# Kernel optimization log

Measured on AMD Instinct MI355X. Metric: run time of the kernel, lower is better.

## Reference

```python
import jax, jax.numpy as jnp
import numpy as np

N = 50000
E = 600000
H = 128
LN_EPS = 1e-5


def _layer_norm(h, g, b):
    mu = jnp.mean(h, axis=-1, keepdims=True)
    var = jnp.var(h, axis=-1, keepdims=True)
    return (h - mu) * jax.lax.rsqrt(var + LN_EPS) * g + b


def _mlp(h, params):
    # params = (w0, b0, w1, b1, w2, b2, ln_g, ln_b); mlp_layers=2 pattern:
    # Linear->ReLU->Linear->ReLU->Linear->LayerNorm
    w0, b0, w1, b1, w2, b2, g, be = params
    h = jax.nn.relu(h @ w0 + b0)
    h = jax.nn.relu(h @ w1 + b1)
    h = h @ w2 + b2
    return _layer_norm(h, g, be)


def setup_inputs() -> dict:
    key = jax.random.key(0)
    ks = jax.random.split(key, 16)
    def lin(k, fan_in, fan_out):
        lim = 1.0 / np.sqrt(fan_in)
        kw, kb = jax.random.split(k)
        w = jax.random.uniform(kw, (fan_in, fan_out), jnp.float32, -lim, lim)
        b = jax.random.uniform(kb, (fan_out,), jnp.float32, -lim, lim)
        return w, b
    x = jax.random.normal(ks[0], (N, H), jnp.float32)
    e = jax.random.normal(ks[1], (E, H), jnp.float32)
    edge_index = jax.random.randint(ks[2], (2, E), 0, N, jnp.int64)
    we0, be0 = lin(ks[3], 3 * H, H)
    we1, be1 = lin(ks[4], H, H)
    we2, be2 = lin(ks[5], H, H)
    wn0, bn0 = lin(ks[6], 2 * H, H)
    wn1, bn1 = lin(ks[7], H, H)
    wn2, bn2 = lin(ks[8], H, H)
    return {
        "x": x, "e": e, "edge_index": edge_index,
        "we0": we0, "be0": be0, "we1": we1, "be1": be1, "we2": we2, "be2": be2,
        "ge": jnp.ones((H,), jnp.float32), "bge": jnp.zeros((H,), jnp.float32),
        "wn0": wn0, "bn0": bn0, "wn1": wn1, "bn1": bn1, "wn2": wn2, "bn2": bn2,
        "gn": jnp.ones((H,), jnp.float32), "bgn": jnp.zeros((H,), jnp.float32),
    }


def reference(x, e, edge_index,
              we0, be0, we1, be1, we2, be2, ge, bge,
              wn0, bn0, wn1, bn1, wn2, bn2, gn, bgn):
    src = edge_index[0]
    dst = edge_index[1]
    # gather node feats per edge -> [E, 3H] -> edge MLP -> [E, H]
    edge_in = jnp.concatenate([x[dst], x[src], e], axis=-1)
    e_new = _mlp(edge_in, (we0, be0, we1, be1, we2, be2, ge, bge))
    # scatter-add edge messages into destination nodes -> [N, H]
    agg = jax.ops.segment_sum(e_new, dst, num_segments=x.shape[0])
    node_in = jnp.concatenate([x, agg], axis=-1)
    x_new = x + _mlp(node_in, (wn0, bn0, wn1, bn1, wn2, bn2, gn, bgn))
    return (x_new, e_new)
```

## Files before the change

kernel.cpp:

```cpp
#include <hip/hip_runtime.h>

#define NN 50000
#define NE 600000
#define HD 128

typedef __attribute__((ext_vector_type(8))) short short8;
typedef __attribute__((ext_vector_type(4))) float floatx4;

__device__ __forceinline__ unsigned short f2bf(float f) {
  unsigned int u = __builtin_bit_cast(unsigned int, f);
  u += 0x7FFFu + ((u >> 16) & 1u);
  return (unsigned short)(u >> 16);
}

__device__ __forceinline__ short8 cvt8(const float* __restrict__ p) {
  floatx4 v0 = *(const floatx4*)p;
  floatx4 v1 = *(const floatx4*)(p + 4);
  short8 r;
  r[0] = (short)f2bf(v0[0]); r[1] = (short)f2bf(v0[1]);
  r[2] = (short)f2bf(v0[2]); r[3] = (short)f2bf(v0[3]);
  r[4] = (short)f2bf(v1[0]); r[5] = (short)f2bf(v1[1]);
  r[6] = (short)f2bf(v1[2]); r[7] = (short)f2bf(v1[3]);
  return r;
}

__global__ void pack_w(const float* __restrict__ w, unsigned short* __restrict__ wp,
                       int total) {
  int p = blockIdx.x * blockDim.x + threadIdx.x;
  if (p >= total) return;
  int j = p & 7, lane = (p >> 3) & 63, t = p >> 9;
  int n0 = t & 7, k0 = t >> 3;
  int k = k0 * 32 + (lane >> 4) * 8 + j;
  int n = n0 * 16 + (lane & 15);
  wp[p] = f2bf(w[k * HD + n]);
}

__global__ void cvt_bf16(const float* __restrict__ in,
                         unsigned short* __restrict__ out, int total8) {
  int p = blockIdx.x * blockDim.x + threadIdx.x;
  if (p >= total8) return;
  short8 r = cvt8(in + (size_t)p * 8);
  *(short8*)(out + (size_t)p * 8) = r;
}

template <int KSTEPS>
__device__ __forceinline__ void gemm_tile(const unsigned short* a_base, int a_stride,
                                          const unsigned short* __restrict__ wp,
                                          int lane, floatx4* acc) {
  int quad = lane >> 4, l16 = lane & 15;
  for (int k0 = 0; k0 < KSTEPS; ++k0) {
    short8 a = *(const short8*)(a_base + l16 * a_stride + k0 * 32 + quad * 8);
    const unsigned short* w = wp + k0 * 4096 + lane * 8;
#pragma unroll
    for (int n0 = 0; n0 < 8; ++n0) {
      short8 b = *(const short8*)(w + n0 * 512);
      acc[n0] = __builtin_amdgcn_mfma_f32_16x16x32_bf16(a, b, acc[n0], 0, 0, 0);
    }
  }
}

__device__ __forceinline__ void store_relu_bf16(const floatx4* acc,
                                                const float* __restrict__ bias,
                                                unsigned short* out_base, int stride,
                                                int lane) {
  int quad = lane >> 4, l16 = lane & 15;
#pragma unroll
  for (int n0 = 0; n0 < 8; ++n0) {
    float bv = bias[n0 * 16 + l16];
#pragma unroll
    for (int r = 0; r < 4; ++r) {
      float v = acc[n0][r] + bv;
      v = v > 0.f ? v : 0.f;
      out_base[(quad * 4 + r) * stride + n0 * 16 + l16] = f2bf(v);
    }
  }
}

#define SH 136

template <int XBF>
__global__ __launch_bounds__(256, 4) void edge_kernel(
    const float* __restrict__ x, const unsigned short* __restrict__ xb,
    const float* __restrict__ e, const int* __restrict__ idx,
    const unsigned short* __restrict__ w0p, const float* __restrict__ b0,
    const unsigned short* __restrict__ w1p, const float* __restrict__ b1,
    const unsigned short* __restrict__ w2p, const float* __restrict__ b2,
    const float* __restrict__ g, const float* __restrict__ bg,
    float* __restrict__ e_out, float* __restrict__ agg) {
  __shared__ __align__(16) unsigned short lh[64 * SH];

  int wave = threadIdx.x >> 6, lane = threadIdx.x & 63;
  int quad = lane >> 4, l16 = lane & 15;
  int ebase = blockIdx.x * 64 + wave * 16;
  int arow = ebase + l16;
  int s = idx[arow], d = idx[NE + arow];

  floatx4 acc[8];
  floatx4 z = {0.f, 0.f, 0.f, 0.f};
#pragma unroll
  for (int t = 0; t < 8; ++t) acc[t] = z;

  const float* ee = e + (size_t)arow * HD + quad * 8;
  if constexpr (XBF) {
    const unsigned short* xd = xb + (size_t)d * HD + quad * 8;
    const unsigned short* xs = xb + (size_t)s * HD + quad * 8;
#pragma unroll
    for (int k0 = 0; k0 < 12; ++k0) {
      short8 a;
      if (k0 < 4)
        a = *(const short8*)(xd + k0 * 32);
      else if (k0 < 8)
        a = *(const short8*)(xs + (k0 - 4) * 32);
      else
        a = cvt8(ee + (k0 - 8) * 32);
      const unsigned short* w = w0p + k0 * 4096 + lane * 8;
#pragma unroll
      for (int n0 = 0; n0 < 8; ++n0) {
        short8 b = *(const short8*)(w + n0 * 512);
        acc[n0] = __builtin_amdgcn_mfma_f32_16x16x32_bf16(a, b, acc[n0], 0, 0, 0);
      }
    }
  } else {
    const float* xd = x + (size_t)d * HD + quad * 8;
    const float* xs = x + (size_t)s * HD + quad * 8;
#pragma unroll
    for (int k0 = 0; k0 < 12; ++k0) {
      short8 a;
      if (k0 < 4)
        a = cvt8(xd + k0 * 32);
      else if (k0 < 8)
        a = cvt8(xs + (k0 - 4) * 32);
      else
        a = cvt8(ee + (k0 - 8) * 32);
      const unsigned short* w = w0p + k0 * 4096 + lane * 8;
#pragma unroll
      for (int n0 = 0; n0 < 8; ++n0) {
        short8 b = *(const short8*)(w + n0 * 512);
        acc[n0] = __builtin_amdgcn_mfma_f32_16x16x32_bf16(a, b, acc[n0], 0, 0, 0);
      }
    }
  }
  unsigned short* lhw = lh + wave * 16 * SH;
  store_relu_bf16(acc, b0, lhw, SH, lane);

#pragma unroll
  for (int t = 0; t < 8; ++t) acc[t] = z;
  gemm_tile<4>(lhw, SH, w1p, lane, acc);
  store_relu_bf16(acc, b1, lhw, SH, lane);

#pragma unroll
  for (int t = 0; t < 8; ++t) acc[t] = z;
  gemm_tile<4>(lhw, SH, w2p, lane, acc);

  float h3[8][4];
#pragma unroll
  for (int n0 = 0; n0 < 8; ++n0) {
    float bv = b2[n0 * 16 + l16];
#pragma unroll
    for (int r = 0; r < 4; ++r) h3[n0][r] = acc[n0][r] + bv;
  }
  float s1[4] = {0.f, 0.f, 0.f, 0.f}, s2[4] = {0.f, 0.f, 0.f, 0.f};
#pragma unroll
  for (int n0 = 0; n0 < 8; ++n0)
#pragma unroll
    for (int r = 0; r < 4; ++r) {
      s1[r] += h3[n0][r];
      s2[r] += h3[n0][r] * h3[n0][r];
    }
#pragma unroll
  for (int m = 1; m < 16; m <<= 1) {
#pragma unroll
    for (int r = 0; r < 4; ++r) {
      s1[r] += __shfl_xor(s1[r], m, 64);
      s2[r] += __shfl_xor(s2[r], m, 64);
    }
  }
  float mu[4], rs[4];
#pragma unroll
  for (int r = 0; r < 4; ++r) {
    mu[r] = s1[r] * (1.f / 128.f);
    float var = s2[r] * (1.f / 128.f) - mu[r] * mu[r];
    rs[r] = rsqrtf(var + 1e-5f);
  }
  int drow[4];
#pragma unroll
  for (int r = 0; r < 4; ++r) drow[r] = idx[NE + ebase + quad * 4 + r];
#pragma unroll
  for (int n0 = 0; n0 < 8; ++n0) {
    int col = n0 * 16 + l16;
    float gv = g[col], bv = bg[col];
#pragma unroll
    for (int r = 0; r < 4; ++r) {
      int ei = ebase + quad * 4 + r;
      float v = (h3[n0][r] - mu[r]) * rs[r] * gv + bv;
      e_out[(size_t)ei * HD + col] = v;
      atomicAdd(&agg[(size_t)drow[r] * HD + col], v);
    }
  }
}

template <int XBF>
__global__ __launch_bounds__(256, 4) void node_kernel(
    const float* __restrict__ x, const unsigned short* __restrict__ xb,
    const float* __restrict__ agg, const unsigned short* __restrict__ w0p,
    const float* __restrict__ b0, const unsigned short* __restrict__ w1p,
    const float* __restrict__ b1, const unsigned short* __restrict__ w2p,
    const float* __restrict__ b2, const float* __restrict__ g,
    const float* __restrict__ bg, float* __restrict__ x_out) {
  __shared__ __align__(16) unsigned short lh[64 * SH];

  int wave = threadIdx.x >> 6, lane = threadIdx.x & 63;
  int quad = lane >> 4, l16 = lane & 15;
  int nbase = blockIdx.x * 64 + wave * 16;
  int arow = nbase + l16;
  int nc = arow < NN ? arow : NN - 1;

  floatx4 acc[8];
  floatx4 z = {0.f, 0.f, 0.f, 0.f};
#pragma unroll
  for (int t = 0; t < 8; ++t) acc[t] = z;

  const float* ar = agg + (size_t)nc * HD + quad * 8;
  if constexpr (XBF) {
    const unsigned short* xr = xb + (size_t)nc * HD + quad * 8;
#pragma unroll
    for (int k0 = 0; k0 < 8; ++k0) {
      short8 a;
      if (k0 < 4)
        a = *(const short8*)(xr + k0 * 32);
      else
        a = cvt8(ar + (k0 - 4) * 32);
      const unsigned short* w = w0p + k0 * 4096 + lane * 8;
#pragma unroll
      for (int n0 = 0; n0 < 8; ++n0) {
        short8 b = *(const short8*)(w + n0 * 512);
        acc[n0] = __builtin_amdgcn_mfma_f32_16x16x32_bf16(a, b, acc[n0], 0, 0, 0);
      }
    }
  } else {
    const float* xr = x + (size_t)nc * HD + quad * 8;
#pragma unroll
    for (int k0 = 0; k0 < 8; ++k0) {
      short8 a;
      if (k0 < 4)
        a = cvt8(xr + k0 * 32);
      else
        a = cvt8(ar + (k0 - 4) * 32);
      const unsigned short* w = w0p + k0 * 4096 + lane * 8;
#pragma unroll
      for (int n0 = 0; n0 < 8; ++n0) {
        short8 b = *(const short8*)(w + n0 * 512);
        acc[n0] = __builtin_amdgcn_mfma_f32_16x16x32_bf16(a, b, acc[n0], 0, 0, 0);
      }
    }
  }
  unsigned short* lhw = lh + wave * 16 * SH;
  store_relu_bf16(acc, b0, lhw, SH, lane);

#pragma unroll
  for (int t = 0; t < 8; ++t) acc[t] = z;
  gemm_tile<4>(lhw, SH, w1p, lane, acc);
  store_relu_bf16(acc, b1, lhw, SH, lane);

#pragma unroll
  for (int t = 0; t < 8; ++t) acc[t] = z;
  gemm_tile<4>(lhw, SH, w2p, lane, acc);

  float h3[8][4];
#pragma unroll
  for (int n0 = 0; n0 < 8; ++n0) {
    float bv = b2[n0 * 16 + l16];
#pragma unroll
    for (int r = 0; r < 4; ++r) h3[n0][r] = acc[n0][r] + bv;
  }
  float s1[4] = {0.f, 0.f, 0.f, 0.f}, s2[4] = {0.f, 0.f, 0.f, 0.f};
#pragma unroll
  for (int n0 = 0; n0 < 8; ++n0)
#pragma unroll
    for (int r = 0; r < 4; ++r) {
      s1[r] += h3[n0][r];
      s2[r] += h3[n0][r] * h3[n0][r];
    }
#pragma unroll
  for (int m = 1; m < 16; m <<= 1) {
#pragma unroll
    for (int r = 0; r < 4; ++r) {
      s1[r] += __shfl_xor(s1[r], m, 64);
      s2[r] += __shfl_xor(s2[r], m, 64);
    }
  }
  float mu[4], rs[4];
#pragma unroll
  for (int r = 0; r < 4; ++r) {
    mu[r] = s1[r] * (1.f / 128.f);
    float var = s2[r] * (1.f / 128.f) - mu[r] * mu[r];
    rs[r] = rsqrtf(var + 1e-5f);
  }
#pragma unroll
  for (int n0 = 0; n0 < 8; ++n0) {
    int col = n0 * 16 + l16;
    float gv = g[col], bv = bg[col];
#pragma unroll
    for (int r = 0; r < 4; ++r) {
      int ni = nbase + quad * 4 + r;
      if (ni < NN) {
        float v = (h3[n0][r] - mu[r]) * rs[r] * gv + bv;
        x_out[(size_t)ni * HD + col] = x[(size_t)ni * HD + col] + v;
      }
    }
  }
}

extern "C" void kernel_launch(void* const* d_in, const int* in_sizes, int n_in,
                              void* d_out, int out_size, void* d_ws, size_t ws_size,
                              hipStream_t stream) {
  const float* x = (const float*)d_in[0];
  const float* e = (const float*)d_in[1];
  const int* idx = (const int*)d_in[2];
  const float* we0 = (const float*)d_in[3];
  const float* be0 = (const float*)d_in[4];
  const float* we1 = (const float*)d_in[5];
  const float* be1 = (const float*)d_in[6];
  const float* we2 = (const float*)d_in[7];
  const float* be2 = (const float*)d_in[8];
  const float* ge = (const float*)d_in[9];
  const float* bge = (const float*)d_in[10];
  const float* wn0 = (const float*)d_in[11];
  const float* bn0 = (const float*)d_in[12];
  const float* wn1 = (const float*)d_in[13];
  const float* bn1 = (const float*)d_in[14];
  const float* wn2 = (const float*)d_in[15];
  const float* bn2 = (const float*)d_in[16];
  const float* gn = (const float*)d_in[17];
  const float* bgn = (const float*)d_in[18];

  float* xout = (float*)d_out;
  float* eout = (float*)d_out + (size_t)NN * HD;

  unsigned short* ws = (unsigned short*)d_ws;
  unsigned short* w0p = ws;
  unsigned short* w1p = w0p + 384 * HD;
  unsigned short* w2p = w1p + HD * HD;
  unsigned short* wn0p = w2p + HD * HD;
  unsigned short* wn1p = wn0p + 256 * HD;
  unsigned short* wn2p = wn1p + HD * HD;
  unsigned short* xb = wn2p + HD * HD;

  size_t w_shorts = (size_t)(384 + 128 + 128 + 256 + 128 + 128) * HD;
  bool use_xb = ws_size >= (w_shorts + (size_t)NN * HD) * sizeof(unsigned short);

  hipMemsetAsync(xout, 0, (size_t)NN * HD * sizeof(float), stream);

  pack_w<<<(384 * HD + 255) / 256, 256, 0, stream>>>(we0, w0p, 384 * HD);
  pack_w<<<(HD * HD + 255) / 256, 256, 0, stream>>>(we1, w1p, HD * HD);
  pack_w<<<(HD * HD + 255) / 256, 256, 0, stream>>>(we2, w2p, HD * HD);
  pack_w<<<(256 * HD + 255) / 256, 256, 0, stream>>>(wn0, wn0p, 256 * HD);
  pack_w<<<(HD * HD + 255) / 256, 256, 0, stream>>>(wn1, wn1p, HD * HD);
  pack_w<<<(HD * HD + 255) / 256, 256, 0, stream>>>(wn2, wn2p, HD * HD);

  if (use_xb) {
    cvt_bf16<<<(NN * HD / 8 + 255) / 256, 256, 0, stream>>>(x, xb, NN * HD / 8);
    edge_kernel<1><<<NE / 64, 256, 0, stream>>>(x, xb, e, idx, w0p, be0, w1p, be1,
                                                w2p, be2, ge, bge, eout, xout);
    node_kernel<1><<<(NN + 63) / 64, 256, 0, stream>>>(
        x, xb, xout, wn0p, bn0, wn1p, bn1, wn2p, bn2, gn, bgn, xout);
  } else {
    edge_kernel<0><<<NE / 64, 256, 0, stream>>>(x, xb, e, idx, w0p, be0, w1p, be1,
                                                w2p, be2, ge, bge, eout, xout);
    node_kernel<0><<<(NN + 63) / 64, 256, 0, stream>>>(
        x, xb, xout, wn0p, bn0, wn1p, bn1, wn2p, bn2, gn, bgn, xout);
  }
}
```

Measured before the change: 990.6 us.

## Replace atomic scatter-add with CSR gather aggregation in node kernel

Builds a destination-sorted CSR (histogram, single-block scan, fill) over the edges. The node kernel then gathers each node's edge messages from e_out and sums them, so the edge kernel no longer issues fp32 atomics into agg and the memset of the output goes away. Weight packing, x conversion and count zeroing are merged into one prep kernel to cut launches. The trade is three extra small kernels, a serial single-block scan, and irregular per-node gather reads of e_out whose cost depends on degree imbalance.

```diff
diff --git a/kernel.cpp b/kernel.cpp
--- a/kernel.cpp
+++ b/kernel.cpp
@@ -6,6 +6,7 @@
 
 typedef __attribute__((ext_vector_type(8))) short short8;
 typedef __attribute__((ext_vector_type(4))) float floatx4;
+typedef __attribute__((ext_vector_type(2))) float floatx2;
 
 __device__ __forceinline__ unsigned short f2bf(float f) {
   unsigned int u = __builtin_bit_cast(unsigned int, f);
@@ -24,10 +25,8 @@
   return r;
 }
 
-__global__ void pack_w(const float* __restrict__ w, unsigned short* __restrict__ wp,
-                       int total) {
-  int p = blockIdx.x * blockDim.x + threadIdx.x;
-  if (p >= total) return;
+__device__ __forceinline__ void pack_one(const float* __restrict__ w,
+                                         unsigned short* __restrict__ wp, int p) {
   int j = p & 7, lane = (p >> 3) & 63, t = p >> 9;
   int n0 = t & 7, k0 = t >> 3;
   int k = k0 * 32 + (lane >> 4) * 8 + j;
@@ -35,12 +34,78 @@
   wp[p] = f2bf(w[k * HD + n]);
 }
 
-__global__ void cvt_bf16(const float* __restrict__ in,
-                         unsigned short* __restrict__ out, int total8) {
-  int p = blockIdx.x * blockDim.x + threadIdx.x;
-  if (p >= total8) return;
-  short8 r = cvt8(in + (size_t)p * 8);
-  *(short8*)(out + (size_t)p * 8) = r;
+__global__ void prep_kernel(const float* __restrict__ we0, const float* __restrict__ we1,
+                            const float* __restrict__ we2, const float* __restrict__ wn0,
+                            const float* __restrict__ wn1, const float* __restrict__ wn2,
+                            unsigned short* __restrict__ wpack,
+                            const float* __restrict__ x, unsigned short* __restrict__ xb,
+                            int* __restrict__ cnt, int do_cnt, int do_cvt) {
+  int p = blockIdx.x * 256 + threadIdx.x;
+  if (p < 147456) {
+    const float* src;
+    int rel;
+    if (p < 49152) { src = we0; rel = p; }
+    else if (p < 65536) { src = we1; rel = p - 49152; }
+    else if (p < 81920) { src = we2; rel = p - 65536; }
+    else if (p < 114688) { src = wn0; rel = p - 81920; }
+    else if (p < 131072) { src = wn1; rel = p - 114688; }
+    else { src = wn2; rel = p - 131072; }
+    pack_one(src, wpack + (p - rel), rel);
+  } else if (p < 197456) {
+    if (do_cnt) cnt[p - 147456] = 0;
+  } else if (p < 997456) {
+    if (do_cvt) {
+      int q = p - 197456;
+      *(short8*)(xb + (size_t)q * 8) = cvt8(x + (size_t)q * 8);
+    }
+  }
+}
+
+__global__ void hist_kernel(const int* __restrict__ idx, int* __restrict__ cnt) {
+  int eid = blockIdx.x * 256 + threadIdx.x;
+  if (eid < NE) atomicAdd(&cnt[idx[NE + eid]], 1);
+}
+
+__global__ __launch_bounds__(1024) void scan_kernel(const int* __restrict__ cnt,
+                                                    int* __restrict__ offs,
+                                                    int* __restrict__ cur) {
+  __shared__ int part[1024];
+  int t = threadIdx.x;
+  int base = t * 49;
+  int s = 0;
+  for (int i = 0; i < 49; ++i) {
+    int g = base + i;
+    if (g < NN) s += cnt[g];
+  }
+  part[t] = s;
+  __syncthreads();
+  for (int off = 1; off < 1024; off <<= 1) {
+    int add = (t >= off) ? part[t - off] : 0;
+    __syncthreads();
+    part[t] += add;
+    __syncthreads();
+  }
+  int run = part[t] - s;
+  for (int i = 0; i < 49; ++i) {
+    int g = base + i;
+    if (g < NN) {
+      int c = cnt[g];
+      offs[g] = run;
+      cur[g] = run;
+      run += c;
+    }
+  }
+  if (t == 1023) offs[NN] = run;
+}
+
+__global__ void fill_kernel(const int* __restrict__ idx, int* __restrict__ cur,
+                            int* __restrict__ perm) {
+  int eid = blockIdx.x * 256 + threadIdx.x;
+  if (eid < NE) {
+    int d = idx[NE + eid];
+    int pos = atomicAdd(&cur[d], 1);
+    perm[pos] = eid;
+  }
 }
 
 template <int KSTEPS>
@@ -78,7 +143,7 @@
 
 #define SH 136
 
-template <int XBF>
+template <int XBF, int ATOM>
 __global__ __launch_bounds__(256, 4) void edge_kernel(
     const float* __restrict__ x, const unsigned short* __restrict__ xb,
     const float* __restrict__ e, const int* __restrict__ idx,
@@ -182,9 +247,6 @@
     float var = s2[r] * (1.f / 128.f) - mu[r] * mu[r];
     rs[r] = rsqrtf(var + 1e-5f);
   }
-  int drow[4];
-#pragma unroll
-  for (int r = 0; r < 4; ++r) drow[r] = idx[NE + ebase + quad * 4 + r];
 #pragma unroll
   for (int n0 = 0; n0 < 8; ++n0) {
     int col = n0 * 16 + l16;
@@ -194,13 +256,143 @@
       int ei = ebase + quad * 4 + r;
       float v = (h3[n0][r] - mu[r]) * rs[r] * gv + bv;
       e_out[(size_t)ei * HD + col] = v;
-      atomicAdd(&agg[(size_t)drow[r] * HD + col], v);
+      if constexpr (ATOM) {
+        int drow = idx[NE + ei];
+        atomicAdd(&agg[(size_t)drow * HD + col], v);
+      }
     }
   }
 }
 
 template <int XBF>
-__global__ __launch_bounds__(256, 4) void node_kernel(
+__global__ __launch_bounds__(256, 4) void node_kernel_csr(
+    const float* __restrict__ x, const unsigned short* __restrict__ xb,
+    const float* __restrict__ e_out, const int* __restrict__ offs,
+    const int* __restrict__ perm, const unsigned short* __restrict__ w0p,
+    const float* __restrict__ b0, const unsigned short* __restrict__ w1p,
+    const float* __restrict__ b1, const unsigned short* __restrict__ w2p,
+    const float* __restrict__ b2, const float* __restrict__ g,
+    const float* __restrict__ bg, float* __restrict__ x_out) {
+  __shared__ __align__(16) unsigned short lh[64 * SH];
+  __shared__ __align__(16) unsigned short sag[64 * SH];
+
+  int wave = threadIdx.x >> 6, lane = threadIdx.x & 63;
+  int quad = lane >> 4, l16 = lane & 15;
+  int nbase = blockIdx.x * 64 + wave * 16;
+
+  unsigned short* sagw = sag + wave * 16 * SH;
+  int c0 = lane * 2;
+  for (int rr = 0; rr < 16; ++rr) {
+    int n = nbase + rr;
+    float a0 = 0.f, a1 = 0.f;
+    if (n < NN) {
+      int beg = offs[n], end = offs[n + 1];
+      int j = beg;
+      for (; j + 4 <= end; j += 4) {
+        int e0 = perm[j], e1 = perm[j + 1], e2 = perm[j + 2], e3 = perm[j + 3];
+        floatx2 v0 = *(const floatx2*)(e_out + (size_t)e0 * HD + c0);
+        floatx2 v1 = *(const floatx2*)(e_out + (size_t)e1 * HD + c0);
+        floatx2 v2 = *(const floatx2*)(e_out + (size_t)e2 * HD + c0);
+        floatx2 v3 = *(const floatx2*)(e_out + (size_t)e3 * HD + c0);
+        a0 += v0[0] + v1[0] + v2[0] + v3[0];
+        a1 += v0[1] + v1[1] + v2[1] + v3[1];
+      }
+      for (; j < end; ++j) {
+        int eid = perm[j];
+        floatx2 v = *(const floatx2*)(e_out + (size_t)eid * HD + c0);
+        a0 += v[0];
+        a1 += v[1];
+      }
+    }
+    unsigned int pk = (unsigned int)f2bf(a0) | ((unsigned int)f2bf(a1) << 16);
+    *(unsigned int*)(sagw + rr * SH + c0) = pk;
+  }
+
+  int arow = nbase + l16;
+  int nc = arow < NN ? arow : NN - 1;
+
+  floatx4 acc[8];
+  floatx4 z = {0.f, 0.f, 0.f, 0.f};
+#pragma unroll
+  for (int t = 0; t < 8; ++t) acc[t] = z;
+
+#pragma unroll
+  for (int k0 = 0; k0 < 8; ++k0) {
+    short8 a;
+    if (k0 < 4) {
+      if constexpr (XBF)
+        a = *(const short8*)(xb + (size_t)nc * HD + quad * 8 + k0 * 32);
+      else
+        a = cvt8(x + (size_t)nc * HD + quad * 8 + k0 * 32);
+    } else {
+      a = *(const short8*)(sagw + l16 * SH + (k0 - 4) * 32 + quad * 8);
+    }
+    const unsigned short* w = w0p + k0 * 4096 + lane * 8;
+#pragma unroll
+    for (int n0 = 0; n0 < 8; ++n0) {
+      short8 b = *(const short8*)(w + n0 * 512);
+      acc[n0] = __builtin_amdgcn_mfma_f32_16x16x32_bf16(a, b, acc[n0], 0, 0, 0);
+    }
+  }
+  unsigned short* lhw = lh + wave * 16 * SH;
+  store_relu_bf16(acc, b0, lhw, SH, lane);
+
+#pragma unroll
+  for (int t = 0; t < 8; ++t) acc[t] = z;
+  gemm_tile<4>(lhw, SH, w1p, lane, acc);
+  store_relu_bf16(acc, b1, lhw, SH, lane);
+
+#pragma unroll
+  for (int t = 0; t < 8; ++t) acc[t] = z;
+  gemm_tile<4>(lhw, SH, w2p, lane, acc);
+
+  float h3[8][4];
+#pragma unroll
+  for (int n0 = 0; n0 < 8; ++n0) {
+    float bv = b2[n0 * 16 + l16];
+#pragma unroll
+    for (int r = 0; r < 4; ++r) h3[n0][r] = acc[n0][r] + bv;
+  }
+  float s1[4] = {0.f, 0.f, 0.f, 0.f}, s2[4] = {0.f, 0.f, 0.f, 0.f};
+#pragma unroll
+  for (int n0 = 0; n0 < 8; ++n0)
+#pragma unroll
+    for (int r = 0; r < 4; ++r) {
+      s1[r] += h3[n0][r];
+      s2[r] += h3[n0][r] * h3[n0][r];
+    }
+#pragma unroll
+  for (int m = 1; m < 16; m <<= 1) {
+#pragma unroll
+    for (int r = 0; r < 4; ++r) {
+      s1[r] += __shfl_xor(s1[r], m, 64);
+      s2[r] += __shfl_xor(s2[r], m, 64);
+    }
+  }
+  float mu[4], rs[4];
+#pragma unroll
+  for (int r = 0; r < 4; ++r) {
+    mu[r] = s1[r] * (1.f / 128.f);
+    float var = s2[r] * (1.f / 128.f) - mu[r] * mu[r];
+    rs[r] = rsqrtf(var + 1e-5f);
+  }
+#pragma unroll
+  for (int n0 = 0; n0 < 8; ++n0) {
+    int col = n0 * 16 + l16;
+    float gv = g[col], bv = bg[col];
+#pragma unroll
+    for (int r = 0; r < 4; ++r) {
+      int ni = nbase + quad * 4 + r;
+      if (ni < NN) {
+        float v = (h3[n0][r] - mu[r]) * rs[r] * gv + bv;
+        x_out[(size_t)ni * HD + col] = x[(size_t)ni * HD + col] + v;
+      }
+    }
+  }
+}
+
+template <int XBF>
+__global__ __launch_bounds__(256, 4) void node_kernel_atom(
     const float* __restrict__ x, const unsigned short* __restrict__ xb,
     const float* __restrict__ agg, const unsigned short* __restrict__ w0p,
     const float* __restrict__ b0, const unsigned short* __restrict__ w1p,
@@ -221,37 +413,22 @@
   for (int t = 0; t < 8; ++t) acc[t] = z;
 
   const float* ar = agg + (size_t)nc * HD + quad * 8;
-  if constexpr (XBF) {
-    const unsigned short* xr = xb + (size_t)nc * HD + quad * 8;
-#pragma unroll
-    for (int k0 = 0; k0 < 8; ++k0) {
-      short8 a;
-      if (k0 < 4)
-        a = *(const short8*)(xr + k0 * 32);
+#pragma unroll
+  for (int k0 = 0; k0 < 8; ++k0) {
+    short8 a;
+    if (k0 < 4) {
+      if constexpr (XBF)
+        a = *(const short8*)(xb + (size_t)nc * HD + quad * 8 + k0 * 32);
       else
-        a = cvt8(ar + (k0 - 4) * 32);
-      const unsigned short* w = w0p + k0 * 4096 + lane * 8;
-#pragma unroll
-      for (int n0 = 0; n0 < 8; ++n0) {
-        short8 b = *(const short8*)(w + n0 * 512);
-        acc[n0] = __builtin_amdgcn_mfma_f32_16x16x32_bf16(a, b, acc[n0], 0, 0, 0);
-      }
-    }
-  } else {
-    const float* xr = x + (size_t)nc * HD + quad * 8;
-#pragma unroll
-    for (int k0 = 0; k0 < 8; ++k0) {
-      short8 a;
-      if (k0 < 4)
-        a = cvt8(xr + k0 * 32);
-      else
-        a = cvt8(ar + (k0 - 4) * 32);
-      const unsigned short* w = w0p + k0 * 4096 + lane * 8;
-#pragma unroll
-      for (int n0 = 0; n0 < 8; ++n0) {
-        short8 b = *(const short8*)(w + n0 * 512);
-        acc[n0] = __builtin_amdgcn_mfma_f32_16x16x32_bf16(a, b, acc[n0], 0, 0, 0);
-      }
+        a = cvt8(x + (size_t)nc * HD + quad * 8 + k0 * 32);
+    } else {
+      a = cvt8(ar + (k0 - 4) * 32);
+    }
+    const unsigned short* w = w0p + k0 * 4096 + lane * 8;
+#pragma unroll
+    for (int n0 = 0; n0 < 8; ++n0) {
+      short8 b = *(const short8*)(w + n0 * 512);
+      acc[n0] = __builtin_amdgcn_mfma_f32_16x16x32_bf16(a, b, acc[n0], 0, 0, 0);
     }
   }
   unsigned short* lhw = lh + wave * 16 * SH;
@@ -337,37 +514,61 @@
   float* xout = (float*)d_out;
   float* eout = (float*)d_out + (size_t)NN * HD;
 
-  unsigned short* ws = (unsigned short*)d_ws;
-  unsigned short* w0p = ws;
-  unsigned short* w1p = w0p + 384 * HD;
-  unsigned short* w2p = w1p + HD * HD;
-  unsigned short* wn0p = w2p + HD * HD;
-  unsigned short* wn1p = wn0p + 256 * HD;
-  unsigned short* wn2p = wn1p + HD * HD;
-  unsigned short* xb = wn2p + HD * HD;
-
-  size_t w_shorts = (size_t)(384 + 128 + 128 + 256 + 128 + 128) * HD;
-  bool use_xb = ws_size >= (w_shorts + (size_t)NN * HD) * sizeof(unsigned short);
-
-  hipMemsetAsync(xout, 0, (size_t)NN * HD * sizeof(float), stream);
-
-  pack_w<<<(384 * HD + 255) / 256, 256, 0, stream>>>(we0, w0p, 384 * HD);
-  pack_w<<<(HD * HD + 255) / 256, 256, 0, stream>>>(we1, w1p, HD * HD);
-  pack_w<<<(HD * HD + 255) / 256, 256, 0, stream>>>(we2, w2p, HD * HD);
-  pack_w<<<(256 * HD + 255) / 256, 256, 0, stream>>>(wn0, wn0p, 256 * HD);
-  pack_w<<<(HD * HD + 255) / 256, 256, 0, stream>>>(wn1, wn1p, HD * HD);
-  pack_w<<<(HD * HD + 255) / 256, 256, 0, stream>>>(wn2, wn2p, HD * HD);
-
-  if (use_xb) {
-    cvt_bf16<<<(NN * HD / 8 + 255) / 256, 256, 0, stream>>>(x, xb, NN * HD / 8);
-    edge_kernel<1><<<NE / 64, 256, 0, stream>>>(x, xb, e, idx, w0p, be0, w1p, be1,
-                                                w2p, be2, ge, bge, eout, xout);
-    node_kernel<1><<<(NN + 63) / 64, 256, 0, stream>>>(
-        x, xb, xout, wn0p, bn0, wn1p, bn1, wn2p, bn2, gn, bgn, xout);
+  const size_t WPK = 147456;
+  const size_t XBN = (size_t)NN * HD;
+  const size_t CSRI = (size_t)NN + (NN + 1) + NN + NE;
+  const size_t WB = WPK * 2, XB = XBN * 2, CSRB = CSRI * 4;
+
+  unsigned short* wpack = (unsigned short*)d_ws;
+  unsigned short* w0p = wpack;
+  unsigned short* w1p = wpack + 49152;
+  unsigned short* w2p = wpack + 65536;
+  unsigned short* wn0p = wpack + 81920;
+  unsigned short* wn1p = wpack + 114688;
+  unsigned short* wn2p = wpack + 131072;
+
+  bool use_csr_xb = ws_size >= WB + XB + CSRB;
+  bool use_csr = use_csr_xb || ws_size >= WB + CSRB;
+  bool use_xb = use_csr_xb || (!use_csr && ws_size >= WB + XB);
+
+  unsigned short* xbuf = wpack + WPK;
+  int* ibase = use_xb ? (int*)(wpack + WPK + XBN) : (int*)(wpack + WPK);
+  int* cnt = ibase;
+  int* offs = cnt + NN;
+  int* cur = offs + NN + 1;
+  int* perm = cur + NN;
+
+  prep_kernel<<<(997456 + 255) / 256, 256, 0, stream>>>(
+      we0, we1, we2, wn0, wn1, wn2, wpack, x, xbuf, cnt, use_csr ? 1 : 0,
+      use_xb ? 1 : 0);
+
+  if (use_csr) {
+    hist_kernel<<<(NE + 255) / 256, 256, 0, stream>>>(idx, cnt);
+    scan_kernel<<<1, 1024, 0, stream>>>(cnt, offs, cur);
+    fill_kernel<<<(NE + 255) / 256, 256, 0, stream>>>(idx, cur, perm);
+    if (use_xb) {
+      edge_kernel<1, 0><<<NE / 64, 256, 0, stream>>>(
+          x, xbuf, e, idx, w0p, be0, w1p, be1, w2p, be2, ge, bge, eout, nullptr);
+      node_kernel_csr<1><<<(NN + 63) / 64, 256, 0, stream>>>(
+          x, xbuf, eout, offs, perm, wn0p, bn0, wn1p, bn1, wn2p, bn2, gn, bgn, xout);
+    } else {
+      edge_kernel<0, 0><<<NE / 64, 256, 0, stream>>>(
+          x, xbuf, e, idx, w0p, be0, w1p, be1, w2p, be2, ge, bge, eout, nullptr);
+      node_kernel_csr<0><<<(NN + 63) / 64, 256, 0, stream>>>(
+          x, xbuf, eout, offs, perm, wn0p, bn0, wn1p, bn1, wn2p, bn2, gn, bgn, xout);
+    }
   } else {
-    edge_kernel<0><<<NE / 64, 256, 0, stream>>>(x, xb, e, idx, w0p, be0, w1p, be1,
-                                                w2p, be2, ge, bge, eout, xout);
-    node_kernel<0><<<(NN + 63) / 64, 256, 0, stream>>>(
-        x, xb, xout, wn0p, bn0, wn1p, bn1, wn2p, bn2, gn, bgn, xout);
-  }
-}
+    hipMemsetAsync(xout, 0, (size_t)NN * HD * sizeof(float), stream);
+    if (use_xb) {
+      edge_kernel<1, 1><<<NE / 64, 256, 0, stream>>>(
+          x, xbuf, e, idx, w0p, be0, w1p, be1, w2p, be2, ge, bge, eout, xout);
+      node_kernel_atom<1><<<(NN + 63) / 64, 256, 0, stream>>>(
+          x, xbuf, xout, wn0p, bn0, wn1p, bn1, wn2p, bn2, gn, bgn, xout);
+    } else {
+      edge_kernel<0, 1><<<NE / 64, 256, 0, stream>>>(
+          x, xbuf, e, idx, w0p, be0, w1p, be1, w2p, be2, ge, bge, eout, xout);
+      node_kernel_atom<0><<<(NN + 63) / 64, 256, 0, stream>>>(
+          x, xbuf, xout, wn0p, bn0, wn1p, bn1, wn2p, bn2, gn, bgn, xout);
+    }
+  }
+}
```

Result: slower. 1.114 ms (+12.4%).
